# Performance work log

Measured on AMD Instinct MI355X. Metric: run time of the kernel, lower is better.

## Reference

```python
import jax, jax.numpy as jnp
import numpy as np

T, B, V, E, H = 128, 32, 32000, 512, 1024
PAD = 0

def setup_inputs() -> dict:
    key = jax.random.key(0)
    ks = jax.random.split(key, 10)
    indices = jax.random.randint(ks[0], (T, B), 0, V)
    emb = jax.random.normal(ks[1], (V, E), jnp.float32) * 0.02
    s = 1.0 / np.sqrt(H).astype(np.float32)
    W_ih = jax.random.normal(ks[2], (4 * H, E), jnp.float32) * s
    W_hh = jax.random.normal(ks[3], (4 * H, H), jnp.float32) * s
    b_ih = jax.random.normal(ks[4], (4 * H,), jnp.float32) * 0.01
    b_hh = jax.random.normal(ks[5], (4 * H,), jnp.float32) * 0.01
    W_out = jax.random.normal(ks[6], (V, H), jnp.float32) * s
    b_out = jnp.zeros((V,), jnp.float32)
    h0 = jax.random.uniform(ks[7], (B, H), jnp.float32, -0.1, 0.1)
    c0 = jax.random.uniform(ks[8], (B, H), jnp.float32, -0.1, 0.1)
    return dict(indices=indices, emb=emb, W_ih=W_ih, W_hh=W_hh,
                b_ih=b_ih, b_hh=b_hh, W_out=W_out, b_out=b_out, h0=h0, c0=c0)

def reference(indices, emb, W_ih, W_hh, b_ih, b_hh, W_out, b_out, h0, c0):
    # embed + relu for all timesteps at once (dropout_rate=0.0 -> identity)
    x_all = jax.nn.relu(emb[indices[:-1]])   # [T-1, B, E]
    targets = indices[1:]                    # [T-1, B]

    def step(carry, inp):
        h, c, loss = carry
        x, tgt = inp
        # torch LSTM gate order: i, f, g, o
        gates = x @ W_ih.T + b_ih + h @ W_hh.T + b_hh   # [B, 4H]
        i, f, g, o = jnp.split(gates, 4, axis=-1)
        c = jax.nn.sigmoid(f) * c + jax.nn.sigmoid(i) * jnp.tanh(g)
        h = jax.nn.sigmoid(o) * jnp.tanh(c)
        logp = jax.nn.log_softmax(h @ W_out.T + b_out, axis=-1)  # [B, V]
        nll = -jnp.take_along_axis(logp, tgt[:, None], axis=-1)[:, 0]
        # NLLLoss(reduction='sum', ignore_index=PAD)
        loss = loss + jnp.sum(jnp.where(tgt != PAD, nll, 0.0))
        return (h, c, loss), None

    (_, _, loss), _ = jax.lax.scan(step, (h0, c0, jnp.float32(0.0)), (x_all, targets))
    return loss
```

## Files before the change

### kernel.cpp

```cpp
#include <hip/hip_runtime.h>
#include <hip/hip_bf16.h>
#include <hip/hip_cooperative_groups.h>
#include <math.h>

namespace cg = cooperative_groups;

typedef __bf16 bf16_t;
typedef bf16_t bf16x8 __attribute__((ext_vector_type(8)));
typedef float f32x4 __attribute__((ext_vector_type(4)));

#define T_SEQ 128
#define NB 32
#define NV 32000
#define NE 512
#define NH 1024
#define G4 4096
#define MROWS 4064
#define MPAD 4096

#define NBLK 256

__device__ __forceinline__ void g2lds16(const bf16_t* g, bf16_t* l) {
  __builtin_amdgcn_global_load_lds((const __attribute__((address_space(1))) void*)g,
                                   (__attribute__((address_space(3))) void*)l, 16, 0, 0);
}

__device__ __forceinline__ unsigned short bf16bits(float x) {
  bf16_t b = (bf16_t)x;
  return __builtin_bit_cast(unsigned short, b);
}

__global__ void k_prep(const int* __restrict__ idx, const float* __restrict__ emb,
                       const float* __restrict__ W_ih, const float* __restrict__ W_hh,
                       const float* __restrict__ b_ih, const float* __restrict__ b_hh,
                       const float* __restrict__ W_out, const float* __restrict__ h0,
                       bf16_t* __restrict__ W_ih_bf, bf16_t* __restrict__ W_hh_bf,
                       bf16_t* __restrict__ W_out_bf, bf16_t* __restrict__ x_bf,
                       bf16_t* __restrict__ h_all, bf16_t* __restrict__ h0_bf,
                       float* __restrict__ bc, float* __restrict__ rowS,
                       int* __restrict__ tgt, unsigned* __restrict__ bar) {
  const long nW_ih = 4096L * 512;
  const long nW_hh = 4096L * 1024;
  const long nW_out = 32000L * 1024;
  const long nX = 4096L * 512;
  const long nH0 = 32L * 1024;
  const long nHpad = 32L * 1024;
  const long NTOTAL = nW_ih + nW_hh + nW_out + nX + nH0 + nHpad + 3 * 4096L + 1024;
  long stride = (long)gridDim.x * blockDim.x;
  for (long i = (long)blockIdx.x * blockDim.x + threadIdx.x; i < NTOTAL; i += stride) {
    long j = i;
    if (j < nW_ih) { W_ih_bf[j] = (bf16_t)W_ih[j]; continue; }
    j -= nW_ih;
    if (j < nW_hh) { W_hh_bf[j] = (bf16_t)W_hh[j]; continue; }
    j -= nW_hh;
    if (j < nW_out) { W_out_bf[j] = (bf16_t)W_out[j]; continue; }
    j -= nW_out;
    if (j < nX) {
      long m = j >> 9; int e = (int)(j & 511);
      float x = 0.f;
      if (m < MROWS) { x = emb[(long)idx[m] * NE + e]; x = x > 0.f ? x : 0.f; }
      x_bf[j] = (bf16_t)x; continue;
    }
    j -= nX;
    if (j < nH0) { h0_bf[j] = (bf16_t)h0[j]; continue; }
    j -= nH0;
    if (j < nHpad) { h_all[4161536L + j] = (bf16_t)0.f; continue; }
    j -= nHpad;
    if (j < 4096) { bc[j] = b_ih[j] + b_hh[j]; continue; }
    j -= 4096;
    if (j < 4096) { rowS[j] = 0.f; continue; }
    j -= 4096;
    if (j < 4096) { tgt[j] = (j < MROWS) ? idx[j + NB] : 0; continue; }
    j -= 4096;
    { bar[j] = 0u; continue; }
  }
}

__global__ __launch_bounds__(256) void k_gemm1(const bf16_t* __restrict__ A,
                                               const bf16_t* __restrict__ B,
                                               const float* __restrict__ bc,
                                               bf16_t* __restrict__ C) {
  const int K = 512;
  int tid = threadIdx.x, wid = tid >> 6, lane = tid & 63;
  int wm = wid & 1, wn = wid >> 1;
  int quad = lane >> 4, l15 = lane & 15;
  int mBase = blockIdx.x * 64, nBase = blockIdx.y * 128;

  const bf16x8* pa0 = (const bf16x8*)(A + (long)(mBase + wm * 32 + l15) * K + quad * 8);
  const bf16x8* pa1 = (const bf16x8*)(A + (long)(mBase + wm * 32 + 16 + l15) * K + quad * 8);
  const bf16x8* pb[4];
#pragma unroll
  for (int j = 0; j < 4; ++j)
    pb[j] = (const bf16x8*)(B + (long)(nBase + wn * 64 + j * 16 + l15) * K + quad * 8);

  f32x4 acc[2][4];
#pragma unroll
  for (int mi = 0; mi < 2; ++mi)
#pragma unroll
    for (int ni = 0; ni < 4; ++ni) acc[mi][ni] = (f32x4){0.f, 0.f, 0.f, 0.f};

  for (int kk = 0; kk < K / 32; ++kk) {
    bf16x8 a0 = pa0[kk * 4], a1 = pa1[kk * 4];
    bf16x8 b0 = pb[0][kk * 4], b1 = pb[1][kk * 4], b2 = pb[2][kk * 4], b3 = pb[3][kk * 4];
    acc[0][0] = __builtin_amdgcn_mfma_f32_16x16x32_bf16(a0, b0, acc[0][0], 0, 0, 0);
    acc[0][1] = __builtin_amdgcn_mfma_f32_16x16x32_bf16(a0, b1, acc[0][1], 0, 0, 0);
    acc[0][2] = __builtin_amdgcn_mfma_f32_16x16x32_bf16(a0, b2, acc[0][2], 0, 0, 0);
    acc[0][3] = __builtin_amdgcn_mfma_f32_16x16x32_bf16(a0, b3, acc[0][3], 0, 0, 0);
    acc[1][0] = __builtin_amdgcn_mfma_f32_16x16x32_bf16(a1, b0, acc[1][0], 0, 0, 0);
    acc[1][1] = __builtin_amdgcn_mfma_f32_16x16x32_bf16(a1, b1, acc[1][1], 0, 0, 0);
    acc[1][2] = __builtin_amdgcn_mfma_f32_16x16x32_bf16(a1, b2, acc[1][2], 0, 0, 0);
    acc[1][3] = __builtin_amdgcn_mfma_f32_16x16x32_bf16(a1, b3, acc[1][3], 0, 0, 0);
  }
#pragma unroll
  for (int ni = 0; ni < 4; ++ni) {
    int col = nBase + wn * 64 + ni * 16 + l15;
    float bcv = bc[col];
#pragma unroll
    for (int mi = 0; mi < 2; ++mi)
#pragma unroll
      for (int r = 0; r < 4; ++r) {
        int row = mBase + wm * 32 + mi * 16 + quad * 4 + r;
        C[(long)row * G4 + col] = (bf16_t)(acc[mi][ni][r] + bcv);
      }
  }
}

__device__ __forceinline__ void lbar(unsigned* grp, unsigned* root, unsigned* gen,
                                     unsigned target) {
  __syncthreads();
  if (threadIdx.x == 0) {
    asm volatile("" ::: "memory");
    __builtin_amdgcn_s_waitcnt(0x0f70);
    unsigned o = __hip_atomic_fetch_add(grp, 1u, __ATOMIC_RELAXED,
                                        __HIP_MEMORY_SCOPE_AGENT);
    if ((o & 15u) == 15u) {
      unsigned r = __hip_atomic_fetch_add(root, 1u, __ATOMIC_RELAXED,
                                          __HIP_MEMORY_SCOPE_AGENT);
      if ((r & 7u) == 7u)
        __hip_atomic_store(gen, (r >> 3) + 1u, __ATOMIC_RELAXED,
                           __HIP_MEMORY_SCOPE_AGENT);
    }
    while (__hip_atomic_load(gen, __ATOMIC_RELAXED, __HIP_MEMORY_SCOPE_AGENT) < target)
      __builtin_amdgcn_s_sleep(1);
    asm volatile("" ::: "memory");
  }
  __syncthreads();
}

__global__ __launch_bounds__(512) void k_rec4(const bf16_t* __restrict__ gates_x,
                                              const bf16_t* __restrict__ W_hh_bf,
                                              const bf16_t* __restrict__ h0_bf,
                                              bf16_t* __restrict__ h_all,
                                              const float* __restrict__ c0,
                                              unsigned* __restrict__ bar) {
  __shared__ float red[2 * 16 * 16 * 4];

  int bid = blockIdx.x;
  int mi = bid & 1;
  int hb = bid >> 1;
  int gbase = hb * 8;
  int tid = threadIdx.x, wid = tid >> 6, lane = tid & 63;
  int cg = wid & 1, kh = wid >> 1;
  int quad = lane >> 4, l15 = lane & 15;

  int wrow = (cg ? 2048 : 0) + ((l15 & 8) ? 1024 : 0) + gbase + (l15 & 7);
  const bf16x8* pw = (const bf16x8*)(W_hh_bf + (long)wrow * NH + kh * 256 + quad * 8);
  bf16x8 wfrag[8];
#pragma unroll
  for (int kk = 0; kk < 8; ++kk) wfrag[kk] = pw[kk * 4];

  unsigned* grp = bar + mi * 512 + (hb & 7) * 32;
  unsigned* root = bar + mi * 512 + 256;
  unsigned* gen = bar + mi * 512 + 288;

  int pb = tid >> 2, pu2 = (tid & 3) * 2;
  int u0 = gbase + pu2;
  int bglob = mi * 16 + pb;
  float cst0 = 0.f, cst1 = 0.f;
  if (tid < 64) {
    cst0 = c0[(long)bglob * NH + u0];
    cst1 = c0[(long)bglob * NH + u0 + 1];
  }
  unsigned* h32 = (unsigned*)h_all;

  for (int t = 0; t < T_SEQ - 1; ++t) {
    unsigned gxi2 = 0, gxf2 = 0, gxg2 = 0, gxo2 = 0;
    if (tid < 64) {
      const unsigned* gp = (const unsigned*)(gates_x + (long)(t * NB + bglob) * G4);
      int q = u0 >> 1;
      gxi2 = gp[q]; gxf2 = gp[512 + q]; gxg2 = gp[1024 + q]; gxo2 = gp[1536 + q];
    }

    const bf16_t* hp = (t == 0) ? h0_bf : (h_all + (long)(t - 1) * NB * NH);
    const bf16x8* pa = (const bf16x8*)(hp + (long)(mi * 16 + l15) * NH + kh * 256 + quad * 8);
    f32x4 acc = (f32x4){0.f, 0.f, 0.f, 0.f};
#pragma unroll
    for (int kk = 0; kk < 8; ++kk) {
      bf16x8 a = pa[kk * 4];
      acc = __builtin_amdgcn_mfma_f32_16x16x32_bf16(a, wfrag[kk], acc, 0, 0, 0);
    }
#pragma unroll
    for (int r = 0; r < 4; ++r) {
      int b = quad * 4 + r;
      red[(((cg << 4) + b) << 6) + (l15 << 2) + kh] = acc[r];
    }
    __syncthreads();

    if (tid < 64) {
      const float4* rp = (const float4*)red;
      float hv[2];
#pragma unroll
      for (int d = 0; d < 2; ++d) {
        int q = pu2 + d;
        float4 vi = rp[(pb << 4) + q];
        float4 vf = rp[(pb << 4) + 8 + q];
        float4 vg = rp[((16 + pb) << 4) + q];
        float4 vo = rp[((16 + pb) << 4) + 8 + q];
        unsigned bi = d ? (gxi2 & 0xffff0000u) : (gxi2 << 16);
        unsigned bff = d ? (gxf2 & 0xffff0000u) : (gxf2 << 16);
        unsigned bg = d ? (gxg2 & 0xffff0000u) : (gxg2 << 16);
        unsigned bo = d ? (gxo2 & 0xffff0000u) : (gxo2 << 16);
        float iv = vi.x + vi.y + vi.z + vi.w + __builtin_bit_cast(float, bi);
        float fv = vf.x + vf.y + vf.z + vf.w + __builtin_bit_cast(float, bff);
        float gv = vg.x + vg.y + vg.z + vg.w + __builtin_bit_cast(float, bg);
        float ov = vo.x + vo.y + vo.z + vo.w + __builtin_bit_cast(float, bo);
        float si = 1.f / (1.f + __expf(-iv));
        float sf = 1.f / (1.f + __expf(-fv));
        float so = 1.f / (1.f + __expf(-ov));
        float tg = 1.f - 2.f / (__expf(2.f * gv) + 1.f);
        float& cs = d ? cst1 : cst0;
        cs = sf * cs + si * tg;
        float th = 1.f - 2.f / (__expf(2.f * cs) + 1.f);
        hv[d] = so * th;
      }
      unsigned pack = (unsigned)bf16bits(hv[0]) | ((unsigned)bf16bits(hv[1]) << 16);
      __hip_atomic_store(&h32[(long)(t * NB + bglob) * 512 + (u0 >> 1)], pack,
                         __ATOMIC_RELAXED, __HIP_MEMORY_SCOPE_AGENT);
    }
    if (t < T_SEQ - 2) lbar(grp, root, gen, (unsigned)(t + 1));
  }
}

__global__ __launch_bounds__(256) void k_gemm2(const bf16_t* __restrict__ A,
                                               const bf16_t* __restrict__ B,
                                               const float* __restrict__ b_out,
                                               float* __restrict__ rowS) {
  __shared__ bf16_t As[128 * 32];
  __shared__ bf16_t Bs[128 * 32];
  const int K = 1024;
  int tid = threadIdx.x, wid = tid >> 6, lane = tid & 63;
  int wm = wid & 1, wn = wid >> 1;
  int quad = lane >> 4, l15 = lane & 15;
  int mBase = blockIdx.x * 128, nBase = blockIdx.y * 128;

  int rc = lane >> 2, seg = lane & 3;
  int cA0 = 2 * wid, cA1 = 2 * wid + 1;
  const bf16_t* gA0 = A + (size_t)(mBase + cA0 * 16 + rc) * K + seg * 8;
  const bf16_t* gA1 = A + (size_t)(mBase + cA1 * 16 + rc) * K + seg * 8;
  const bf16_t* gB0 = B + (size_t)(nBase + cA0 * 16 + rc) * K + seg * 8;
  const bf16_t* gB1 = B + (size_t)(nBase + cA1 * 16 + rc) * K + seg * 8;
  bf16_t* lA0 = As + cA0 * 512;
  bf16_t* lA1 = As + cA1 * 512;
  bf16_t* lB0 = Bs + cA0 * 512;
  bf16_t* lB1 = Bs + cA1 * 512;

  const bf16x8* pa[4];
  const bf16x8* pbf[4];
#pragma unroll
  for (int i = 0; i < 4; ++i) {
    pa[i] = (const bf16x8*)(As + (wm * 64 + i * 16 + l15) * 32 + quad * 8);
    pbf[i] = (const bf16x8*)(Bs + (wn * 64 + i * 16 + l15) * 32 + quad * 8);
  }

  f32x4 acc[4][4];
#pragma unroll
  for (int i = 0; i < 4; ++i)
#pragma unroll
    for (int j = 0; j < 4; ++j) acc[i][j] = (f32x4){0.f, 0.f, 0.f, 0.f};

  for (int kt = 0; kt < K / 32; ++kt) {
    g2lds16(gA0 + kt * 32, lA0);
    g2lds16(gA1 + kt * 32, lA1);
    g2lds16(gB0 + kt * 32, lB0);
    g2lds16(gB1 + kt * 32, lB1);
    __syncthreads();

    bf16x8 af[4], bf[4];
#pragma unroll
    for (int i = 0; i < 4; ++i) { af[i] = *pa[i]; bf[i] = *pbf[i]; }
#pragma unroll
    for (int i = 0; i < 4; ++i)
#pragma unroll
      for (int j = 0; j < 4; ++j)
        acc[i][j] = __builtin_amdgcn_mfma_f32_16x16x32_bf16(af[i], bf[j], acc[i][j], 0, 0, 0);
    __syncthreads();
  }

#pragma unroll
  for (int i = 0; i < 4; ++i) {
    float rs[4] = {0.f, 0.f, 0.f, 0.f};
#pragma unroll
    for (int j = 0; j < 4; ++j) {
      int col = nBase + wn * 64 + j * 16 + l15;
      float bb = b_out[col];
#pragma unroll
      for (int r = 0; r < 4; ++r) rs[r] += __expf(acc[i][j][r] + bb);
    }
#pragma unroll
    for (int r = 0; r < 4; ++r) {
#pragma unroll
      for (int s = 1; s < 16; s <<= 1) rs[r] += __shfl_xor(rs[r], s);
      if (l15 == 0) {
        int row = mBase + wm * 64 + i * 16 + quad * 4 + r;
        if (row < MROWS) atomicAdd(&rowS[row], rs[r]);
      }
    }
  }
}

__global__ __launch_bounds__(256) void k_tgt(const bf16_t* __restrict__ h_all,
                                             const bf16_t* __restrict__ W_out_bf,
                                             const float* __restrict__ b_out,
                                             const int* __restrict__ tgt,
                                             float* __restrict__ tgt_logit) {
  int gw = (int)((blockIdx.x * blockDim.x + threadIdx.x) >> 6);
  int lane = threadIdx.x & 63;
  if (gw >= MROWS) return;
  int v = tgt[gw];
  const bf16x8* ph = (const bf16x8*)(h_all + (long)gw * NH + lane * 16);
  const bf16x8* pw = (const bf16x8*)(W_out_bf + (long)v * NH + lane * 16);
  float acc = 0.f;
#pragma unroll
  for (int j = 0; j < 2; ++j) {
    bf16x8 h8 = ph[j], w8 = pw[j];
#pragma unroll
    for (int q = 0; q < 8; ++q) acc += (float)h8[q] * (float)w8[q];
  }
#pragma unroll
  for (int s = 1; s < 64; s <<= 1) acc += __shfl_xor(acc, s);
  if (lane == 0) tgt_logit[gw] = acc + b_out[v];
}

__global__ __launch_bounds__(256) void k_loss(const float* __restrict__ rowS,
                                              const float* __restrict__ tl,
                                              const int* __restrict__ tgt,
                                              float* __restrict__ out) {
  __shared__ float sm[256];
  float s = 0.f;
  for (int i = threadIdx.x; i < MROWS; i += 256)
    if (tgt[i] != 0) s += logf(rowS[i]) - tl[i];
  sm[threadIdx.x] = s;
  __syncthreads();
  for (int off = 128; off > 0; off >>= 1) {
    if (threadIdx.x < off) sm[threadIdx.x] += sm[threadIdx.x + off];
    __syncthreads();
  }
  if (threadIdx.x == 0) out[0] = sm[0];
}

extern "C" void kernel_launch(void* const* d_in, const int* in_sizes, int n_in,
                              void* d_out, int out_size, void* d_ws, size_t ws_size,
                              hipStream_t stream) {
  const int* idx = (const int*)d_in[0];
  const float* emb = (const float*)d_in[1];
  const float* W_ih = (const float*)d_in[2];
  const float* W_hh = (const float*)d_in[3];
  const float* b_ih = (const float*)d_in[4];
  const float* b_hh = (const float*)d_in[5];
  const float* W_out = (const float*)d_in[6];
  const float* b_out = (const float*)d_in[7];
  const float* h0 = (const float*)d_in[8];
  const float* c0 = (const float*)d_in[9];

  char* ws = (char*)d_ws;
  bf16_t* W_ih_bf = (bf16_t*)ws;            ws += 4096L * 512 * 2;
  bf16_t* W_hh_bf = (bf16_t*)ws;            ws += 4096L * 1024 * 2;
  bf16_t* W_out_bf = (bf16_t*)ws;           ws += 32000L * 1024 * 2;
  bf16_t* x_bf = (bf16_t*)ws;               ws += 4096L * 512 * 2;
  bf16_t* gates_x = (bf16_t*)ws;            ws += 4096L * 4096 * 2;
  bf16_t* h_all = (bf16_t*)ws;              ws += 4096L * 1024 * 2;
  bf16_t* h0_bf = (bf16_t*)ws;              ws += 32L * 1024 * 2;
  float* bc = (float*)ws;                   ws += 4096L * 4;
  float* rowS = (float*)ws;                 ws += 4096L * 4;
  float* tgt_logit = (float*)ws;            ws += 4096L * 4;
  int* tgt = (int*)ws;                      ws += 4096L * 4;
  unsigned* bar = (unsigned*)ws;            ws += 1024L * 4;

  k_prep<<<4096, 256, 0, stream>>>(idx, emb, W_ih, W_hh, b_ih, b_hh, W_out, h0,
                                   W_ih_bf, W_hh_bf, W_out_bf, x_bf, h_all, h0_bf,
                                   bc, rowS, tgt, bar);

  k_gemm1<<<dim3(64, 32), 256, 0, stream>>>(x_bf, W_ih_bf, bc, gates_x);

  {
    void* args[] = {(void*)&gates_x, (void*)&W_hh_bf, (void*)&h0_bf, (void*)&h_all,
                    (void*)&c0, (void*)&bar};
    hipLaunchCooperativeKernel((void*)k_rec4, dim3(NBLK), dim3(512), args, 0, stream);
  }

  k_gemm2<<<dim3(32, 250), 256, 0, stream>>>(h_all, W_out_bf, b_out, rowS);

  k_tgt<<<1016, 256, 0, stream>>>(h_all, W_out_bf, b_out, tgt, tgt_logit);

  k_loss<<<1, 256, 0, stream>>>(rowS, tgt_logit, tgt, (float*)d_out);
}
```

Baseline: 1.331 ms.

## Replace hierarchical atomic grid barrier with per-block progress flags in LSTM recurrence

Drops the two-level atomic-counter barrier. Each block now publishes a per-timestep progress flag after storing its h slice, and wave 0 of every block polls all 128 flags of its batch half with coherent dwordx2 loads before reading the previous h. The h fragment loads are also hoisted, and the MFMA chain is split into two independent accumulators to shorten the dependency chain. This removes serialized atomic round trips on the critical path of every step. In exchange, 64 lanes per block spin on global memory, and correctness depends on the flag store becoming visible only after the h stores.

```diff
diff --git a/kernel.cpp b/kernel.cpp
--- a/kernel.cpp
+++ b/kernel.cpp
@@ -8,6 +8,7 @@
 typedef __bf16 bf16_t;
 typedef bf16_t bf16x8 __attribute__((ext_vector_type(8)));
 typedef float f32x4 __attribute__((ext_vector_type(4)));
+typedef unsigned u32x2 __attribute__((ext_vector_type(2)));
 
 #define T_SEQ 128
 #define NB 32
@@ -125,34 +126,12 @@
   }
 }
 
-__device__ __forceinline__ void lbar(unsigned* grp, unsigned* root, unsigned* gen,
-                                     unsigned target) {
-  __syncthreads();
-  if (threadIdx.x == 0) {
-    asm volatile("" ::: "memory");
-    __builtin_amdgcn_s_waitcnt(0x0f70);
-    unsigned o = __hip_atomic_fetch_add(grp, 1u, __ATOMIC_RELAXED,
-                                        __HIP_MEMORY_SCOPE_AGENT);
-    if ((o & 15u) == 15u) {
-      unsigned r = __hip_atomic_fetch_add(root, 1u, __ATOMIC_RELAXED,
-                                          __HIP_MEMORY_SCOPE_AGENT);
-      if ((r & 7u) == 7u)
-        __hip_atomic_store(gen, (r >> 3) + 1u, __ATOMIC_RELAXED,
-                           __HIP_MEMORY_SCOPE_AGENT);
-    }
-    while (__hip_atomic_load(gen, __ATOMIC_RELAXED, __HIP_MEMORY_SCOPE_AGENT) < target)
-      __builtin_amdgcn_s_sleep(1);
-    asm volatile("" ::: "memory");
-  }
-  __syncthreads();
-}
-
-__global__ __launch_bounds__(512) void k_rec4(const bf16_t* __restrict__ gates_x,
+__global__ __launch_bounds__(512) void k_rec5(const bf16_t* __restrict__ gates_x,
                                               const bf16_t* __restrict__ W_hh_bf,
                                               const bf16_t* __restrict__ h0_bf,
                                               bf16_t* __restrict__ h_all,
                                               const float* __restrict__ c0,
-                                              unsigned* __restrict__ bar) {
+                                              unsigned* __restrict__ flags) {
   __shared__ float red[2 * 16 * 16 * 4];
 
   int bid = blockIdx.x;
@@ -169,10 +148,6 @@
 #pragma unroll
   for (int kk = 0; kk < 8; ++kk) wfrag[kk] = pw[kk * 4];
 
-  unsigned* grp = bar + mi * 512 + (hb & 7) * 32;
-  unsigned* root = bar + mi * 512 + 256;
-  unsigned* gen = bar + mi * 512 + 288;
-
   int pb = tid >> 2, pu2 = (tid & 3) * 2;
   int u0 = gbase + pu2;
   int bglob = mi * 16 + pb;
@@ -182,6 +157,7 @@
     cst1 = c0[(long)bglob * NH + u0 + 1];
   }
   unsigned* h32 = (unsigned*)h_all;
+  const unsigned* fp = flags + mi * 128 + (lane << 1);
 
   for (int t = 0; t < T_SEQ - 1; ++t) {
     unsigned gxi2 = 0, gxf2 = 0, gxg2 = 0, gxo2 = 0;
@@ -191,14 +167,31 @@
       gxi2 = gp[q]; gxf2 = gp[512 + q]; gxg2 = gp[1024 + q]; gxo2 = gp[1536 + q];
     }
 
+    if (t > 0 && wid == 0) {
+      u32x2 fv;
+      while (1) {
+        asm volatile("global_load_dwordx2 %0, %1, off sc0 sc1\n\t"
+                     "s_waitcnt vmcnt(0)"
+                     : "=&v"(fv) : "v"(fp) : "memory");
+        int ok = (fv.x >= (unsigned)t) & (fv.y >= (unsigned)t);
+        if (__all(ok)) break;
+      }
+    }
+    __syncthreads();
+
     const bf16_t* hp = (t == 0) ? h0_bf : (h_all + (long)(t - 1) * NB * NH);
     const bf16x8* pa = (const bf16x8*)(hp + (long)(mi * 16 + l15) * NH + kh * 256 + quad * 8);
-    f32x4 acc = (f32x4){0.f, 0.f, 0.f, 0.f};
-#pragma unroll
-    for (int kk = 0; kk < 8; ++kk) {
-      bf16x8 a = pa[kk * 4];
-      acc = __builtin_amdgcn_mfma_f32_16x16x32_bf16(a, wfrag[kk], acc, 0, 0, 0);
-    }
+    bf16x8 hfr[8];
+#pragma unroll
+    for (int kk = 0; kk < 8; ++kk) hfr[kk] = pa[kk * 4];
+    f32x4 acc0 = (f32x4){0.f, 0.f, 0.f, 0.f};
+    f32x4 acc1 = (f32x4){0.f, 0.f, 0.f, 0.f};
+#pragma unroll
+    for (int kk = 0; kk < 4; ++kk) {
+      acc0 = __builtin_amdgcn_mfma_f32_16x16x32_bf16(hfr[kk], wfrag[kk], acc0, 0, 0, 0);
+      acc1 = __builtin_amdgcn_mfma_f32_16x16x32_bf16(hfr[kk + 4], wfrag[kk + 4], acc1, 0, 0, 0);
+    }
+    f32x4 acc = acc0 + acc1;
 #pragma unroll
     for (int r = 0; r < 4; ++r) {
       int b = quad * 4 + r;
@@ -236,8 +229,13 @@
       unsigned pack = (unsigned)bf16bits(hv[0]) | ((unsigned)bf16bits(hv[1]) << 16);
       __hip_atomic_store(&h32[(long)(t * NB + bglob) * 512 + (u0 >> 1)], pack,
                          __ATOMIC_RELAXED, __HIP_MEMORY_SCOPE_AGENT);
-    }
-    if (t < T_SEQ - 2) lbar(grp, root, gen, (unsigned)(t + 1));
+      asm volatile("" ::: "memory");
+      __builtin_amdgcn_s_waitcnt(0x0f70);
+      asm volatile("" ::: "memory");
+      if (tid == 0)
+        __hip_atomic_store(&flags[mi * 128 + hb], (unsigned)(t + 1),
+                           __ATOMIC_RELAXED, __HIP_MEMORY_SCOPE_AGENT);
+    }
   }
 }
 
@@ -395,7 +393,7 @@
   {
     void* args[] = {(void*)&gates_x, (void*)&W_hh_bf, (void*)&h0_bf, (void*)&h_all,
                     (void*)&c0, (void*)&bar};
-    hipLaunchCooperativeKernel((void*)k_rec4, dim3(NBLK), dim3(512), args, 0, stream);
+    hipLaunchCooperativeKernel((void*)k_rec5, dim3(NBLK), dim3(512), args, 0, stream);
   }
 
   k_gemm2<<<dim3(32, 250), 256, 0, stream>>>(h_all, W_out_bf, b_out, rowS);
```

After: 1.471 ms. 1.11x slower.

## Replace per-step grid barrier with fine-grained dataflow counters in LSTM recurrence

Applied to the files above, without the earlier changes.

The hierarchical grid barrier in the recurrent kernel is replaced by per-slice counters: each block increments the counter for its hidden-unit slice after storing h, and each wave waits only on the counters covering the K-slice it reads. The reduction buffer is double-buffered by timestep and padded to a 68-float stride, which removes the trailing __syncthreads and reduces LDS bank conflicts. This shortens the critical path per timestep, at the cost of relying on relaxed atomics and waitcnt ordering for the h visibility guarantees.

```diff
diff --git a/kernel.cpp b/kernel.cpp
--- a/kernel.cpp
+++ b/kernel.cpp
@@ -125,35 +125,13 @@
   }
 }
 
-__device__ __forceinline__ void lbar(unsigned* grp, unsigned* root, unsigned* gen,
-                                     unsigned target) {
-  __syncthreads();
-  if (threadIdx.x == 0) {
-    asm volatile("" ::: "memory");
-    __builtin_amdgcn_s_waitcnt(0x0f70);
-    unsigned o = __hip_atomic_fetch_add(grp, 1u, __ATOMIC_RELAXED,
-                                        __HIP_MEMORY_SCOPE_AGENT);
-    if ((o & 15u) == 15u) {
-      unsigned r = __hip_atomic_fetch_add(root, 1u, __ATOMIC_RELAXED,
-                                          __HIP_MEMORY_SCOPE_AGENT);
-      if ((r & 7u) == 7u)
-        __hip_atomic_store(gen, (r >> 3) + 1u, __ATOMIC_RELAXED,
-                           __HIP_MEMORY_SCOPE_AGENT);
-    }
-    while (__hip_atomic_load(gen, __ATOMIC_RELAXED, __HIP_MEMORY_SCOPE_AGENT) < target)
-      __builtin_amdgcn_s_sleep(1);
-    asm volatile("" ::: "memory");
-  }
-  __syncthreads();
-}
-
-__global__ __launch_bounds__(512) void k_rec4(const bf16_t* __restrict__ gates_x,
+__global__ __launch_bounds__(512) void k_rec6(const bf16_t* __restrict__ gates_x,
                                               const bf16_t* __restrict__ W_hh_bf,
                                               const bf16_t* __restrict__ h0_bf,
                                               bf16_t* __restrict__ h_all,
                                               const float* __restrict__ c0,
                                               unsigned* __restrict__ bar) {
-  __shared__ float red[2 * 16 * 16 * 4];
+  __shared__ __align__(16) float red[2][32 * 68];
 
   int bid = blockIdx.x;
   int mi = bid & 1;
@@ -169,9 +147,8 @@
 #pragma unroll
   for (int kk = 0; kk < 8; ++kk) wfrag[kk] = pw[kk * 4];
 
-  unsigned* grp = bar + mi * 512 + (hb & 7) * 32;
-  unsigned* root = bar + mi * 512 + 256;
-  unsigned* gen = bar + mi * 512 + 288;
+  unsigned* cellp = bar + mi * 512 + (2 * kh + (lane & 1)) * 32;
+  unsigned* mycell = bar + mi * 512 + (hb >> 4) * 32;
 
   int pb = tid >> 2, pu2 = (tid & 3) * 2;
   int u0 = gbase + pu2;
@@ -191,6 +168,13 @@
       gxi2 = gp[q]; gxf2 = gp[512 + q]; gxg2 = gp[1024 + q]; gxo2 = gp[1536 + q];
     }
 
+    if (t > 0 && lane < 2) {
+      unsigned need = 16u * (unsigned)t;
+      while (__hip_atomic_load(cellp, __ATOMIC_RELAXED, __HIP_MEMORY_SCOPE_AGENT) < need)
+        __builtin_amdgcn_s_sleep(1);
+    }
+    asm volatile("" ::: "memory");
+
     const bf16_t* hp = (t == 0) ? h0_bf : (h_all + (long)(t - 1) * NB * NH);
     const bf16x8* pa = (const bf16x8*)(hp + (long)(mi * 16 + l15) * NH + kh * 256 + quad * 8);
     f32x4 acc = (f32x4){0.f, 0.f, 0.f, 0.f};
@@ -199,23 +183,24 @@
       bf16x8 a = pa[kk * 4];
       acc = __builtin_amdgcn_mfma_f32_16x16x32_bf16(a, wfrag[kk], acc, 0, 0, 0);
     }
+    float* rb = red[t & 1];
 #pragma unroll
     for (int r = 0; r < 4; ++r) {
-      int b = quad * 4 + r;
-      red[(((cg << 4) + b) << 6) + (l15 << 2) + kh] = acc[r];
+      int row = (cg << 4) + (quad << 2) + r;
+      rb[row * 68 + (l15 << 2) + kh] = acc[r];
     }
     __syncthreads();
 
     if (tid < 64) {
-      const float4* rp = (const float4*)red;
+      const float* rc = red[t & 1];
       float hv[2];
 #pragma unroll
       for (int d = 0; d < 2; ++d) {
         int q = pu2 + d;
-        float4 vi = rp[(pb << 4) + q];
-        float4 vf = rp[(pb << 4) + 8 + q];
-        float4 vg = rp[((16 + pb) << 4) + q];
-        float4 vo = rp[((16 + pb) << 4) + 8 + q];
+        float4 vi = *(const float4*)(rc + pb * 68 + (q << 2));
+        float4 vf = *(const float4*)(rc + pb * 68 + ((8 + q) << 2));
+        float4 vg = *(const float4*)(rc + (16 + pb) * 68 + (q << 2));
+        float4 vo = *(const float4*)(rc + (16 + pb) * 68 + ((8 + q) << 2));
         unsigned bi = d ? (gxi2 & 0xffff0000u) : (gxi2 << 16);
         unsigned bff = d ? (gxf2 & 0xffff0000u) : (gxf2 << 16);
         unsigned bg = d ? (gxg2 & 0xffff0000u) : (gxg2 << 16);
@@ -236,8 +221,15 @@
       unsigned pack = (unsigned)bf16bits(hv[0]) | ((unsigned)bf16bits(hv[1]) << 16);
       __hip_atomic_store(&h32[(long)(t * NB + bglob) * 512 + (u0 >> 1)], pack,
                          __ATOMIC_RELAXED, __HIP_MEMORY_SCOPE_AGENT);
-    }
-    if (t < T_SEQ - 2) lbar(grp, root, gen, (unsigned)(t + 1));
+      if (t < T_SEQ - 2) {
+        asm volatile("" ::: "memory");
+        __builtin_amdgcn_s_waitcnt(0x0f70);
+        asm volatile("" ::: "memory");
+        if (tid == 0)
+          __hip_atomic_fetch_add(mycell, 1u, __ATOMIC_RELAXED,
+                                 __HIP_MEMORY_SCOPE_AGENT);
+      }
+    }
   }
 }
 
@@ -395,7 +387,7 @@
   {
     void* args[] = {(void*)&gates_x, (void*)&W_hh_bf, (void*)&h0_bf, (void*)&h_all,
                     (void*)&c0, (void*)&bar};
-    hipLaunchCooperativeKernel((void*)k_rec4, dim3(NBLK), dim3(512), args, 0, stream);
+    hipLaunchCooperativeKernel((void*)k_rec6, dim3(NBLK), dim3(512), args, 0, stream);
   }
 
   k_gemm2<<<dim3(32, 250), 256, 0, stream>>>(h_all, W_out_bf, b_out, rowS);
```

Measured after the change: 1.468 ms. 10.3% more time.
